# Optimization experiments

Measured on AMD Instinct MI355X. Metric: run time of the kernel, lower is better.

## Reference

```python
import jax, jax.numpy as jnp
import numpy as np

B, A, N_IN, N_HID, N_OUT, MAX_Z = 2048, 96, 128, 64, 1, 100
SHIFT = float(np.log(2.0))

def ssp(x):
    # shifted softplus: softplus(x) - log(2)
    return jax.nn.softplus(x) - SHIFT

def setup_inputs() -> dict:
    key = jax.random.key(0)
    ks = jax.random.split(key, 8)
    rep = jax.random.normal(ks[0], (B, A, N_IN), dtype=jnp.float32)
    atomic_numbers = jax.random.randint(ks[1], (B, A), 0, MAX_Z)
    atom_mask = jnp.ones((B, A), dtype=jnp.float32)
    s1 = 1.0 / np.sqrt(N_IN)
    s2 = 1.0 / np.sqrt(N_HID)
    W1 = jax.random.uniform(ks[2], (N_IN, N_HID), jnp.float32, -s1, s1)
    b1 = jax.random.uniform(ks[3], (N_HID,), jnp.float32, -s1, s1)
    W2 = jax.random.uniform(ks[4], (N_HID, N_OUT), jnp.float32, -s2, s2)
    b2 = jax.random.uniform(ks[5], (N_OUT,), jnp.float32, -s2, s2)
    atomref_table = jax.random.normal(ks[6], (MAX_Z, N_OUT), dtype=jnp.float32) * 0.1
    atomref_table = atomref_table.at[0].set(0.0)  # mask-atom reference is zero
    mean = jnp.array([0.0], dtype=jnp.float32)
    stddev = jnp.array([1.0], dtype=jnp.float32)
    return {"representation": rep, "atomic_numbers": atomic_numbers,
            "atom_mask": atom_mask, "W1": W1, "b1": b1, "W2": W2, "b2": b2,
            "atomref_table": atomref_table, "mean": mean, "stddev": stddev}

def reference(representation, atomic_numbers, atom_mask, W1, b1, W2, b2,
              atomref_table, mean, stddev):
    # per-atom MLP: [B,A,n_in] -> [B,A,n_out]
    h = ssp(jnp.einsum('bai,ih->bah', representation, W1) + b1)
    yi = jnp.einsum('bah,ho->bao', h, W2) + b2
    # standardize (ScaleShift): y * stddev + mean
    yi = yi * stddev + mean
    # atomref embedding lookup and add
    yi = yi + atomref_table[atomic_numbers]  # [B,A,n_out]
    # masked sum aggregation over atoms (Aggregate axis=1, mean=False)
    y = jnp.sum(yi * atom_mask[..., None], axis=1)  # [B,n_out]
    return y
```

## Files before the change

### kernel.cpp

```cpp
#include <hip/hip_runtime.h>
#include <hip/hip_bf16.h>

#define BB 2048
#define AA 96
#define NIN 128
#define NHID 64

typedef __attribute__((ext_vector_type(8))) short bf16x8;
typedef __attribute__((ext_vector_type(4))) float f32x4;

static __device__ __forceinline__ unsigned short f2bf(float x) {
    unsigned u = __builtin_bit_cast(unsigned, x);
    return (unsigned short)((u + 0x7FFFu + ((u >> 16) & 1u)) >> 16);
}
static __device__ __forceinline__ unsigned cvt_pk_hw(float a, float b) {
    __hip_bfloat162 h = __float22bfloat162_rn(make_float2(a, b));
    unsigned u; __builtin_memcpy(&u, &h, 4);
    return u;
}

__global__ void prep_kernel(const float* __restrict__ w1,
                            const float* __restrict__ b1,
                            const float* __restrict__ w2,
                            unsigned char* __restrict__ ws) {
    const int gid = blockIdx.x * 256 + threadIdx.x;
    if (gid < 1024) {
        const int lane = gid & 63, st = gid >> 6;
        const int s = st >> 2, t = st & 3;
        const int k0 = s * 32 + (lane >> 4) * 8;
        const int n  = t * 16 + (lane & 15);
        unsigned short o[8];
        #pragma unroll
        for (int j = 0; j < 8; ++j) o[j] = f2bf(w1[(k0 + j) * NHID + n]);
        uint4 v; __builtin_memcpy(&v, o, 16);
        ((uint4*)ws)[gid] = v;
    } else if (gid < 1088) {
        ((float*)(ws + 16384))[gid - 1024] = b1[gid - 1024];
    } else if (gid < 1152) {
        ((float*)(ws + 16640))[gid - 1088] = w2[gid - 1088];
    }
}

__global__ __launch_bounds__(256) void atomwise_kernel(
    const float* __restrict__ rep,
    const int*   __restrict__ zs,
    const float* __restrict__ mask,
    const unsigned char* __restrict__ ws,
    const float* __restrict__ b2,
    const float* __restrict__ aref,
    const float* __restrict__ mean,
    const float* __restrict__ stddev,
    float* __restrict__ out)
{
    __shared__ unsigned char smem[16896];

    const int tid  = threadIdx.x;
    const int lane = tid & 63;
    const int wv   = tid >> 6;
    const int nl   = lane & 15;
    const int quad = lane >> 4;
    const int atom0 = (blockIdx.x * 4 + wv) * 16;

    const float* rowp = rep + (size_t)(atom0 + nl) * NIN + quad * 8;
    float4 q[8];
    #pragma unroll
    for (int s = 0; s < 4; ++s) {
        q[2 * s]     = *(const float4*)(rowp + s * 32);
        q[2 * s + 1] = *(const float4*)(rowp + s * 32 + 4);
    }

    const int   ag    = atom0 + quad * 4 + (nl & 3);
    const float mq    = mask[ag];
    const float arefv = aref[zs[ag]];

    {
        const uint4* src = (const uint4*)ws;
        uint4*       dst = (uint4*)smem;
        #pragma unroll
        for (int i = 0; i < 4; ++i) dst[tid + i * 256] = src[tid + i * 256];
        if (tid < 32) dst[1024 + tid] = src[1024 + tid];
    }
    __syncthreads();

    const bf16x8* w1f = (const bf16x8*)smem;
    const float*  b1s = (const float*)(smem + 16384);
    const float*  w2s = (const float*)(smem + 16640);

    const float sdv  = stddev[0];
    const float cadd = fmaf(b2[0], sdv, mean[0]);
    const float LOG2E = 1.4426950408889634f;
    const float LN2   = 0.6931471805599453f;

    f32x4 acc[4];
    #pragma unroll
    for (int t = 0; t < 4; ++t) acc[t] = (f32x4){0.f, 0.f, 0.f, 0.f};

    #pragma unroll
    for (int s = 0; s < 4; ++s) {
        union { bf16x8 v; unsigned u[4]; } fa;
        fa.u[0] = cvt_pk_hw(q[2 * s].x,     q[2 * s].y);
        fa.u[1] = cvt_pk_hw(q[2 * s].z,     q[2 * s].w);
        fa.u[2] = cvt_pk_hw(q[2 * s + 1].x, q[2 * s + 1].y);
        fa.u[3] = cvt_pk_hw(q[2 * s + 1].z, q[2 * s + 1].w);
        const bf16x8* fr = &w1f[s * 256 + lane];
        #pragma unroll
        for (int t = 0; t < 4; ++t)
            acc[t] = __builtin_amdgcn_mfma_f32_16x16x32_bf16(fa.v, fr[t * 64], acc[t], 0, 0, 0);
    }

    float v[4];
    #pragma unroll
    for (int r = 0; r < 4; ++r) {
        float p = 0.f;
        #pragma unroll
        for (int t = 0; t < 4; ++t) {
            float x  = acc[t][r] + b1s[t * 16 + nl];
            float ax = fabsf(x);
            float em = exp2f(-ax * LOG2E);
            float sp = fmaxf(x, 0.f) + log2f(1.f + em) * LN2;
            p = fmaf(sp - LN2, w2s[t * 16 + nl], p);
        }
        p += __shfl_xor(p, 1); p += __shfl_xor(p, 2);
        p += __shfl_xor(p, 4); p += __shfl_xor(p, 8);
        v[r] = p;
    }

    const int rsel = nl & 3;
    float vr = v[0];
    vr = rsel == 1 ? v[1] : vr;
    vr = rsel == 2 ? v[2] : vr;
    vr = rsel == 3 ? v[3] : vr;
    float contrib = (nl < 4) ? mq * (fmaf(vr, sdv, cadd) + arefv) : 0.f;
    #pragma unroll
    for (int off = 32; off; off >>= 1) contrib += __shfl_xor(contrib, off);
    if (lane == 0) atomicAdd(out + atom0 / AA, contrib);
}

extern "C" void kernel_launch(void* const* d_in, const int* in_sizes, int n_in,
                              void* d_out, int out_size, void* d_ws, size_t ws_size,
                              hipStream_t stream) {
    const float* rep    = (const float*)d_in[0];
    const int*   zs     = (const int*)  d_in[1];
    const float* mask   = (const float*)d_in[2];
    const float* w1     = (const float*)d_in[3];
    const float* b1     = (const float*)d_in[4];
    const float* w2     = (const float*)d_in[5];
    const float* b2     = (const float*)d_in[6];
    const float* aref   = (const float*)d_in[7];
    const float* mean   = (const float*)d_in[8];
    const float* stddev = (const float*)d_in[9];
    float* out = (float*)d_out;
    unsigned char* ws = (unsigned char*)d_ws;

    (void)hipMemsetAsync(out, 0, (size_t)out_size * sizeof(float), stream);

    prep_kernel<<<dim3(5), dim3(256), 0, stream>>>(w1, b1, w2, ws);

    const int blocks = (BB * AA) / (4 * 16);
    atomwise_kernel<<<dim3(blocks), dim3(256), 0, stream>>>(
        rep, zs, mask, ws, b2, aref, mean, stddev, out);
}
```

Baseline: 163.4 us.

## Stream rep tiles via global_load_lds with per-wave prefetch across four tiles

Each wave now processes four 16-atom tiles instead of one, so there are a quarter as many blocks and the LDS weight copy is amortised. Rep rows are loaded asynchronously into a per-wave 8KB LDS buffer with global_load_lds using an XOR swizzle. The next tile is prefetched once the current tile has been read into registers. The larger LDS footprint per block lowers occupancy, and the single buffer with full waitcnt limits how much memory traffic is in flight per wave.

```diff
diff --git a/kernel.cpp b/kernel.cpp
--- a/kernel.cpp
+++ b/kernel.cpp
@@ -5,9 +5,12 @@
 #define AA 96
 #define NIN 128
 #define NHID 64
+#define MI 4
 
 typedef __attribute__((ext_vector_type(8))) short bf16x8;
 typedef __attribute__((ext_vector_type(4))) float f32x4;
+typedef __attribute__((address_space(1))) const unsigned g_u32;
+typedef __attribute__((address_space(3))) unsigned l_u32;
 
 static __device__ __forceinline__ unsigned short f2bf(float x) {
     unsigned u = __builtin_bit_cast(unsigned, x);
@@ -52,26 +55,16 @@
     const float* __restrict__ stddev,
     float* __restrict__ out)
 {
-    __shared__ unsigned char smem[16896];
+    __shared__ __align__(16) unsigned char smem[49664];
 
     const int tid  = threadIdx.x;
     const int lane = tid & 63;
     const int wv   = tid >> 6;
     const int nl   = lane & 15;
     const int quad = lane >> 4;
-    const int atom0 = (blockIdx.x * 4 + wv) * 16;
 
-    const float* rowp = rep + (size_t)(atom0 + nl) * NIN + quad * 8;
-    float4 q[8];
-    #pragma unroll
-    for (int s = 0; s < 4; ++s) {
-        q[2 * s]     = *(const float4*)(rowp + s * 32);
-        q[2 * s + 1] = *(const float4*)(rowp + s * 32 + 4);
-    }
-
-    const int   ag    = atom0 + quad * 4 + (nl & 3);
-    const float mq    = mask[ag];
-    const float arefv = aref[zs[ag]];
+    unsigned char* mybuf = smem + 16896 + wv * 8192;
+    const int wave_atom0 = (blockIdx.x * 4 + wv) * (16 * MI);
 
     {
         const uint4* src = (const uint4*)ws;
@@ -79,6 +72,23 @@
         #pragma unroll
         for (int i = 0; i < 4; ++i) dst[tid + i * 256] = src[tid + i * 256];
         if (tid < 32) dst[1024 + tid] = src[1024 + tid];
+    }
+
+    float mqs[MI], arefs[MI];
+    #pragma unroll
+    for (int mt = 0; mt < MI; ++mt) {
+        const int ag = wave_atom0 + mt * 16 + quad * 4 + (nl & 3);
+        mqs[mt]   = mask[ag];
+        arefs[mt] = aref[zs[ag]];
+    }
+
+    {
+        const unsigned* gsrc = (const unsigned*)(rep + (size_t)wave_atom0 * NIN);
+        #pragma unroll
+        for (int d = 0; d < 8; ++d)
+            __builtin_amdgcn_global_load_lds(
+                (g_u32*)(gsrc + d * 256 + ((lane ^ d) << 2)),
+                (l_u32*)(mybuf + d * 1024), 16, 0, 0);
     }
     __syncthreads();
 
@@ -91,49 +101,74 @@
     const float LOG2E = 1.4426950408889634f;
     const float LN2   = 0.6931471805599453f;
 
-    f32x4 acc[4];
-    #pragma unroll
-    for (int t = 0; t < 4; ++t) acc[t] = (f32x4){0.f, 0.f, 0.f, 0.f};
+    const int dbase = nl >> 1;
+    const unsigned char* rdbase = mybuf + dbase * 1024;
+    const int gb = ((nl & 1) << 5) | (quad << 1);
 
     #pragma unroll
-    for (int s = 0; s < 4; ++s) {
-        union { bf16x8 v; unsigned u[4]; } fa;
-        fa.u[0] = cvt_pk_hw(q[2 * s].x,     q[2 * s].y);
-        fa.u[1] = cvt_pk_hw(q[2 * s].z,     q[2 * s].w);
-        fa.u[2] = cvt_pk_hw(q[2 * s + 1].x, q[2 * s + 1].y);
-        fa.u[3] = cvt_pk_hw(q[2 * s + 1].z, q[2 * s + 1].w);
-        const bf16x8* fr = &w1f[s * 256 + lane];
+    for (int mt = 0; mt < MI; ++mt) {
+        const int atom0 = wave_atom0 + mt * 16;
+
+        __builtin_amdgcn_s_waitcnt(0);
+
+        union { bf16x8 v; unsigned u[4]; } fa[4];
         #pragma unroll
-        for (int t = 0; t < 4; ++t)
-            acc[t] = __builtin_amdgcn_mfma_f32_16x16x32_bf16(fa.v, fr[t * 64], acc[t], 0, 0, 0);
+        for (int s = 0; s < 4; ++s) {
+            const int g0 = gb + 8 * s;
+            const float4 f0 = *(const float4*)(rdbase + (((g0    ) ^ dbase) << 4));
+            const float4 f1 = *(const float4*)(rdbase + (((g0 + 1) ^ dbase) << 4));
+            fa[s].u[0] = cvt_pk_hw(f0.x, f0.y);
+            fa[s].u[1] = cvt_pk_hw(f0.z, f0.w);
+            fa[s].u[2] = cvt_pk_hw(f1.x, f1.y);
+            fa[s].u[3] = cvt_pk_hw(f1.z, f1.w);
+        }
+
+        if (mt + 1 < MI) {
+            const unsigned* gsrc = (const unsigned*)(rep + (size_t)(atom0 + 16) * NIN);
+            #pragma unroll
+            for (int d = 0; d < 8; ++d)
+                __builtin_amdgcn_global_load_lds(
+                    (g_u32*)(gsrc + d * 256 + ((lane ^ d) << 2)),
+                    (l_u32*)(mybuf + d * 1024), 16, 0, 0);
+        }
+
+        f32x4 acc[4];
+        #pragma unroll
+        for (int t = 0; t < 4; ++t) acc[t] = (f32x4){0.f, 0.f, 0.f, 0.f};
+        #pragma unroll
+        for (int s = 0; s < 4; ++s) {
+            const bf16x8* fr = &w1f[s * 256 + lane];
+            #pragma unroll
+            for (int t = 0; t < 4; ++t)
+                acc[t] = __builtin_amdgcn_mfma_f32_16x16x32_bf16(fa[s].v, fr[t * 64], acc[t], 0, 0, 0);
+        }
+
+        float v[4];
+        #pragma unroll
+        for (int r = 0; r < 4; ++r) {
+            float p = 0.f;
+            #pragma unroll
+            for (int t = 0; t < 4; ++t) {
+                float x  = acc[t][r] + b1s[t * 16 + nl];
+                float ax = fabsf(x);
+                float em = exp2f(-ax * LOG2E);
+                float sp = fmaxf(x, 0.f) + log2f(1.f + em) * LN2;
+                p = fmaf(sp - LN2, w2s[t * 16 + nl], p);
+            }
+            p += __shfl_xor(p, 1); p += __shfl_xor(p, 2);
+            p += __shfl_xor(p, 4); p += __shfl_xor(p, 8);
+            v[r] = p;
+        }
+        const int rsel = nl & 3;
+        float vr = v[0];
+        vr = rsel == 1 ? v[1] : vr;
+        vr = rsel == 2 ? v[2] : vr;
+        vr = rsel == 3 ? v[3] : vr;
+        float contrib = (nl < 4) ? mqs[mt] * (fmaf(vr, sdv, cadd) + arefs[mt]) : 0.f;
+        #pragma unroll
+        for (int off = 32; off; off >>= 1) contrib += __shfl_xor(contrib, off);
+        if (lane == 0) atomicAdd(out + atom0 / AA, contrib);
     }
-
-    float v[4];
-    #pragma unroll
-    for (int r = 0; r < 4; ++r) {
-        float p = 0.f;
-        #pragma unroll
-        for (int t = 0; t < 4; ++t) {
-            float x  = acc[t][r] + b1s[t * 16 + nl];
-            float ax = fabsf(x);
-            float em = exp2f(-ax * LOG2E);
-            float sp = fmaxf(x, 0.f) + log2f(1.f + em) * LN2;
-            p = fmaf(sp - LN2, w2s[t * 16 + nl], p);
-        }
-        p += __shfl_xor(p, 1); p += __shfl_xor(p, 2);
-        p += __shfl_xor(p, 4); p += __shfl_xor(p, 8);
-        v[r] = p;
-    }
-
-    const int rsel = nl & 3;
-    float vr = v[0];
-    vr = rsel == 1 ? v[1] : vr;
-    vr = rsel == 2 ? v[2] : vr;
-    vr = rsel == 3 ? v[3] : vr;
-    float contrib = (nl < 4) ? mq * (fmaf(vr, sdv, cadd) + arefv) : 0.f;
-    #pragma unroll
-    for (int off = 32; off; off >>= 1) contrib += __shfl_xor(contrib, off);
-    if (lane == 0) atomicAdd(out + atom0 / AA, contrib);
 }
 
 extern "C" void kernel_launch(void* const* d_in, const int* in_sizes, int n_in,
@@ -156,7 +191,7 @@
 
     prep_kernel<<<dim3(5), dim3(256), 0, stream>>>(w1, b1, w2, ws);
 
-    const int blocks = (BB * AA) / (4 * 16);
+    const int blocks = (BB * AA) / (4 * 16 * MI);
     atomwise_kernel<<<dim3(blocks), dim3(256), 0, stream>>>(
         rep, zs, mask, ws, b2, aref, mean, stddev, out);
 }
```

New measurement: 167.3 us. 2.4% more time.
